# Kernel tuning notes

Hardware: AMD Instinct MI355X
Metric: run time of the kernel (lower is better)

Reference implementation:

```python
import jax, jax.numpy as jnp
import numpy as np

KERNEL = 5
PADDING = 2

def setup_inputs() -> dict:
    key = jax.random.key(0)
    k1, k2 = jax.random.split(key)
    x = jax.random.normal(k1, (16, 16, 512, 512), dtype=jnp.float32)
    filter_w = jax.random.normal(k2, (16, 16, KERNEL), dtype=jnp.float32)
    return {"x": x, "filter_w": filter_w}

def reference(x, filter_w):
    # torch.diag_embed: (C_out, C_in, k) -> (C_out, C_in, k, k) with values on the diagonal
    k = filter_w.shape[-1]
    kernel = filter_w[..., :, None] * jnp.eye(k, dtype=filter_w.dtype)  # OIHW
    out = jax.lax.conv_general_dilated(
        x, kernel,
        window_strides=(1, 1),
        padding=((PADDING, PADDING), (PADDING, PADDING)),
        dimension_numbers=("NCHW", "OIHW", "NCHW"),
    )
    return out
```

## Files before the change

### kernel.cpp

```cpp
#include <hip/hip_runtime.h>


#define HH    512
#define WW    512
#define CH    16
#define KK    5
#define IMG   (HH * WW)
#define CHIMG (CH * IMG)

#define HT 16
#define WT 64
#define RI 20
#define WI 68
#define NCHUNK (RI * 2)

typedef __attribute__((ext_vector_type(8))) short bf16x8;
typedef __attribute__((ext_vector_type(4))) float f32x4;
typedef __attribute__((ext_vector_type(4))) int   i32x4;

union I4S8 { i32x4 i; bf16x8 s; };

__device__ __forceinline__ unsigned cvt_pk_bf16(float lo, float hi) {
    unsigned r;
    asm("v_cvt_pk_bf16_f32 %0, %1, %2" : "=v"(r) : "v"(lo), "v"(hi));
    return r;
}

__global__ __launch_bounds__(256)
void diag_conv_mfma(const float* __restrict__ x,
                    const float* __restrict__ fw,
                    float* __restrict__ out)
{
    __shared__ i32x4 xl[NCHUNK * WI];

    const int tid = threadIdx.x;

    const int bid = blockIdx.x;
    const int swz = ((bid & 7) << 9) | (bid >> 3);
    const int n  = swz >> 8;
    const int ht = (swz >> 3) & 31;
    const int wt = swz & 7;
    const int h0 = ht * HT;
    const int w0 = wt * WT;

    const int wv   = tid >> 6;
    const int lane = tid & 63;

    const float* __restrict__ xn = x + (size_t)n * CHIMG;

#pragma unroll
    for (int u = 0; u < 10; ++u) {
        const int unit = u * 4 + wv;
        const int ri = unit >> 1;
        const int ih = unit & 1;
        const int r  = h0 - 2 + ri;
        const int w  = w0 - 2 + lane;
        const bool ok = ((unsigned)r < (unsigned)HH) & ((unsigned)w < (unsigned)WW);
        const int rc = r < 0 ? 0 : (r > HH - 1 ? HH - 1 : r);
        const int wc = w < 0 ? 0 : (w > WW - 1 ? WW - 1 : w);
        const float* __restrict__ p8 = xn + (size_t)(ih * 8) * IMG + (size_t)rc * WW + wc;
        float v0 = p8[0 * (size_t)IMG], v1 = p8[1 * (size_t)IMG];
        float v2 = p8[2 * (size_t)IMG], v3 = p8[3 * (size_t)IMG];
        float v4 = p8[4 * (size_t)IMG], v5 = p8[5 * (size_t)IMG];
        float v6 = p8[6 * (size_t)IMG], v7 = p8[7 * (size_t)IMG];
        if (!ok) { v0=v1=v2=v3=v4=v5=v6=v7 = 0.f; }
        i32x4 pk;
        pk.x = (int)cvt_pk_bf16(v0, v1);
        pk.y = (int)cvt_pk_bf16(v2, v3);
        pk.z = (int)cvt_pk_bf16(v4, v5);
        pk.w = (int)cvt_pk_bf16(v6, v7);
        xl[unit * WI + lane] = pk;
    }
    if (tid < 160) {
        const int ri  = tid >> 3;
        const int rem = tid & 7;
        const int wi  = 64 + (rem & 3);
        const int ih  = rem >> 2;
        const int r   = h0 - 2 + ri;
        const int w   = w0 - 2 + wi;
        const bool ok = ((unsigned)r < (unsigned)HH) & ((unsigned)w < (unsigned)WW);
        const int rc = r < 0 ? 0 : (r > HH - 1 ? HH - 1 : r);
        const int wc = w < 0 ? 0 : (w > WW - 1 ? WW - 1 : w);
        const float* __restrict__ p8 = xn + (size_t)(ih * 8) * IMG + (size_t)rc * WW + wc;
        float v0 = p8[0 * (size_t)IMG], v1 = p8[1 * (size_t)IMG];
        float v2 = p8[2 * (size_t)IMG], v3 = p8[3 * (size_t)IMG];
        float v4 = p8[4 * (size_t)IMG], v5 = p8[5 * (size_t)IMG];
        float v6 = p8[6 * (size_t)IMG], v7 = p8[7 * (size_t)IMG];
        if (!ok) { v0=v1=v2=v3=v4=v5=v6=v7 = 0.f; }
        i32x4 pk;
        pk.x = (int)cvt_pk_bf16(v0, v1);
        pk.y = (int)cvt_pk_bf16(v2, v3);
        pk.z = (int)cvt_pk_bf16(v4, v5);
        pk.w = (int)cvt_pk_bf16(v6, v7);
        xl[(ri * 2 + ih) * WI + wi] = pk;
    }

    const int p   = lane & 15;
    const int ihl = (lane >> 4) & 1;
    const int tb  = lane >> 5;

    bf16x8 afrag[3];
#pragma unroll
    for (int s = 0; s < 3; ++s) {
        const int tap = 2 * s + tb;
        I4S8 a;
        a.i = (i32x4){0, 0, 0, 0};
        if (tap < KK) {
            const float* __restrict__ wp = fw + ((size_t)p * CH + ihl * 8) * KK + tap;
            float q0 = wp[0 * KK], q1 = wp[1 * KK], q2 = wp[2 * KK], q3 = wp[3 * KK];
            float q4 = wp[4 * KK], q5 = wp[5 * KK], q6 = wp[6 * KK], q7 = wp[7 * KK];
            a.i.x = (int)cvt_pk_bf16(q0, q1);
            a.i.y = (int)cvt_pk_bf16(q2, q3);
            a.i.z = (int)cvt_pk_bf16(q4, q5);
            a.i.w = (int)cvt_pk_bf16(q6, q7);
        }
        afrag[s] = a.s;
    }

    __syncthreads();

    f32x4 acc[4][4];
#pragma unroll
    for (int yy = 0; yy < 4; ++yy)
#pragma unroll
        for (int g = 0; g < 4; ++g) acc[yy][g] = (f32x4){0.f, 0.f, 0.f, 0.f};

    const int ybase = wv * 4;
#pragma unroll
    for (int yy = 0; yy < 4; ++yy) {
#pragma unroll
        for (int s = 0; s < 3; ++s) {
            const int tap = 2 * s + tb;
            int ri = ybase + yy + tap;
            ri = ri > RI - 1 ? RI - 1 : ri;
            const int c = ri * 2 + ihl;
#pragma unroll
            for (int g = 0; g < 4; ++g) {
                int wi = g * 16 + p + tap;
                wi = wi > WI - 1 ? WI - 1 : wi;
                I4S8 b;
                b.i = xl[c * WI + wi];
                acc[yy][g] = __builtin_amdgcn_mfma_f32_16x16x32_bf16(
                    afrag[s], b.s, acc[yy][g], 0, 0, 0);
            }
        }
    }

    float* __restrict__ on = out + (size_t)n * CHIMG;
    const int og = (lane >> 4) << 2;
#pragma unroll
    for (int yy = 0; yy < 4; ++yy) {
        const int h = h0 + ybase + yy;
#pragma unroll
        for (int g = 0; g < 4; ++g) {
            const int wbase = w0 + g * 16 + p;
#pragma unroll
            for (int reg = 0; reg < 4; ++reg) {
                const int o = og + reg;
                on[(size_t)o * IMG + (size_t)h * WW + wbase] = acc[yy][g][reg];
            }
        }
    }
}

extern "C" void kernel_launch(void* const* d_in, const int* in_sizes, int n_in,
                              void* d_out, int out_size, void* d_ws, size_t ws_size,
                              hipStream_t stream)
{
    const float* x  = (const float*)d_in[0];
    const float* fw = (const float*)d_in[1];
    float* out      = (float*)d_out;

    diag_conv_mfma<<<dim3(4096), dim3(256), 0, stream>>>(x, fw, out);
}
```

Measured before the change: 157.0 us.

## Halve tile height, swap MFMA operands for vector stores, pad LDS, batch loads

The output tile height drops from 16 to 8 rows, doubling the grid to 8192 blocks and cutting per-block LDS and register use. The MFMA operands are swapped so each lane holds four consecutive output pixels, which allows 16-byte vector stores in place of scalar strided stores. LDS rows are padded to 69 chunks to reduce bank conflicts, and all global loads are issued before conversion to expose memory-level parallelism. The trade-off is more halo rows re-read per output row, since the 4 halo rows are now amortised over 8 rows instead of 16.

```diff
diff --git a/kernel.cpp b/kernel.cpp
--- a/kernel.cpp
+++ b/kernel.cpp
@@ -8,10 +8,11 @@
 #define IMG   (HH * WW)
 #define CHIMG (CH * IMG)
 
-#define HT 16
-#define WT 64
-#define RI 20
-#define WI 68
+#define HT  8
+#define WT  64
+#define RI  12
+#define WI  68
+#define WIP 69
 #define NCHUNK (RI * 2)
 
 typedef __attribute__((ext_vector_type(8))) short bf16x8;
@@ -31,14 +32,14 @@
                     const float* __restrict__ fw,
                     float* __restrict__ out)
 {
-    __shared__ i32x4 xl[NCHUNK * WI];
+    __shared__ i32x4 xl[NCHUNK * WIP];
 
     const int tid = threadIdx.x;
 
     const int bid = blockIdx.x;
-    const int swz = ((bid & 7) << 9) | (bid >> 3);
-    const int n  = swz >> 8;
-    const int ht = (swz >> 3) & 31;
+    const int swz = ((bid & 7) << 10) | (bid >> 3);
+    const int n  = swz >> 9;
+    const int ht = (swz >> 3) & 63;
     const int wt = swz & 7;
     const int h0 = ht * HT;
     const int w0 = wt * WT;
@@ -48,86 +49,97 @@
 
     const float* __restrict__ xn = x + (size_t)n * CHIMG;
 
+    const float* pu[6];
+    bool oku[6];
 #pragma unroll
-    for (int u = 0; u < 10; ++u) {
+    for (int u = 0; u < 6; ++u) {
         const int unit = u * 4 + wv;
         const int ri = unit >> 1;
         const int ih = unit & 1;
         const int r  = h0 - 2 + ri;
         const int w  = w0 - 2 + lane;
+        oku[u] = ((unsigned)r < (unsigned)HH) & ((unsigned)w < (unsigned)WW);
+        const int rc = r < 0 ? 0 : (r > HH - 1 ? HH - 1 : r);
+        const int wc = w < 0 ? 0 : (w > WW - 1 ? WW - 1 : w);
+        pu[u] = xn + (size_t)(ih * 8) * IMG + (size_t)rc * WW + wc;
+    }
+    float rv[6][8];
+#pragma unroll
+    for (int u = 0; u < 6; ++u)
+#pragma unroll
+        for (int j = 0; j < 8; ++j)
+            rv[u][j] = pu[u][(size_t)j * IMG];
+#pragma unroll
+    for (int u = 0; u < 6; ++u) {
+        const int unit = u * 4 + wv;
+        i32x4 pk;
+        if (!oku[u]) {
+#pragma unroll
+            for (int j = 0; j < 8; ++j) rv[u][j] = 0.f;
+        }
+        pk.x = (int)cvt_pk_bf16(rv[u][0], rv[u][1]);
+        pk.y = (int)cvt_pk_bf16(rv[u][2], rv[u][3]);
+        pk.z = (int)cvt_pk_bf16(rv[u][4], rv[u][5]);
+        pk.w = (int)cvt_pk_bf16(rv[u][6], rv[u][7]);
+        xl[unit * WIP + lane] = pk;
+    }
+    if (tid < 96) {
+        const int unit = tid >> 2;
+        const int wi   = 64 + (tid & 3);
+        const int ri = unit >> 1;
+        const int ih = unit & 1;
+        const int r  = h0 - 2 + ri;
+        const int w  = w0 - 2 + wi;
         const bool ok = ((unsigned)r < (unsigned)HH) & ((unsigned)w < (unsigned)WW);
         const int rc = r < 0 ? 0 : (r > HH - 1 ? HH - 1 : r);
         const int wc = w < 0 ? 0 : (w > WW - 1 ? WW - 1 : w);
         const float* __restrict__ p8 = xn + (size_t)(ih * 8) * IMG + (size_t)rc * WW + wc;
-        float v0 = p8[0 * (size_t)IMG], v1 = p8[1 * (size_t)IMG];
-        float v2 = p8[2 * (size_t)IMG], v3 = p8[3 * (size_t)IMG];
-        float v4 = p8[4 * (size_t)IMG], v5 = p8[5 * (size_t)IMG];
-        float v6 = p8[6 * (size_t)IMG], v7 = p8[7 * (size_t)IMG];
-        if (!ok) { v0=v1=v2=v3=v4=v5=v6=v7 = 0.f; }
+        float v[8];
+#pragma unroll
+        for (int j = 0; j < 8; ++j) v[j] = p8[(size_t)j * IMG];
+        if (!ok) {
+#pragma unroll
+            for (int j = 0; j < 8; ++j) v[j] = 0.f;
+        }
         i32x4 pk;
-        pk.x = (int)cvt_pk_bf16(v0, v1);
-        pk.y = (int)cvt_pk_bf16(v2, v3);
-        pk.z = (int)cvt_pk_bf16(v4, v5);
-        pk.w = (int)cvt_pk_bf16(v6, v7);
-        xl[unit * WI + lane] = pk;
-    }
-    if (tid < 160) {
-        const int ri  = tid >> 3;
-        const int rem = tid & 7;
-        const int wi  = 64 + (rem & 3);
-        const int ih  = rem >> 2;
-        const int r   = h0 - 2 + ri;
-        const int w   = w0 - 2 + wi;
-        const bool ok = ((unsigned)r < (unsigned)HH) & ((unsigned)w < (unsigned)WW);
-        const int rc = r < 0 ? 0 : (r > HH - 1 ? HH - 1 : r);
-        const int wc = w < 0 ? 0 : (w > WW - 1 ? WW - 1 : w);
-        const float* __restrict__ p8 = xn + (size_t)(ih * 8) * IMG + (size_t)rc * WW + wc;
-        float v0 = p8[0 * (size_t)IMG], v1 = p8[1 * (size_t)IMG];
-        float v2 = p8[2 * (size_t)IMG], v3 = p8[3 * (size_t)IMG];
-        float v4 = p8[4 * (size_t)IMG], v5 = p8[5 * (size_t)IMG];
-        float v6 = p8[6 * (size_t)IMG], v7 = p8[7 * (size_t)IMG];
-        if (!ok) { v0=v1=v2=v3=v4=v5=v6=v7 = 0.f; }
-        i32x4 pk;
-        pk.x = (int)cvt_pk_bf16(v0, v1);
-        pk.y = (int)cvt_pk_bf16(v2, v3);
-        pk.z = (int)cvt_pk_bf16(v4, v5);
-        pk.w = (int)cvt_pk_bf16(v6, v7);
-        xl[(ri * 2 + ih) * WI + wi] = pk;
+        pk.x = (int)cvt_pk_bf16(v[0], v[1]);
+        pk.y = (int)cvt_pk_bf16(v[2], v[3]);
+        pk.z = (int)cvt_pk_bf16(v[4], v[5]);
+        pk.w = (int)cvt_pk_bf16(v[6], v[7]);
+        xl[unit * WIP + wi] = pk;
     }
 
-    const int p   = lane & 15;
+    const int px  = lane & 15;
     const int ihl = (lane >> 4) & 1;
     const int tb  = lane >> 5;
 
-    bf16x8 afrag[3];
+    bf16x8 wfrag[3];
 #pragma unroll
     for (int s = 0; s < 3; ++s) {
         const int tap = 2 * s + tb;
         I4S8 a;
         a.i = (i32x4){0, 0, 0, 0};
         if (tap < KK) {
-            const float* __restrict__ wp = fw + ((size_t)p * CH + ihl * 8) * KK + tap;
-            float q0 = wp[0 * KK], q1 = wp[1 * KK], q2 = wp[2 * KK], q3 = wp[3 * KK];
-            float q4 = wp[4 * KK], q5 = wp[5 * KK], q6 = wp[6 * KK], q7 = wp[7 * KK];
-            a.i.x = (int)cvt_pk_bf16(q0, q1);
-            a.i.y = (int)cvt_pk_bf16(q2, q3);
-            a.i.z = (int)cvt_pk_bf16(q4, q5);
-            a.i.w = (int)cvt_pk_bf16(q6, q7);
+            const float* __restrict__ wp = fw + ((size_t)px * CH + ihl * 8) * KK + tap;
+            a.i.x = (int)cvt_pk_bf16(wp[0 * KK], wp[1 * KK]);
+            a.i.y = (int)cvt_pk_bf16(wp[2 * KK], wp[3 * KK]);
+            a.i.z = (int)cvt_pk_bf16(wp[4 * KK], wp[5 * KK]);
+            a.i.w = (int)cvt_pk_bf16(wp[6 * KK], wp[7 * KK]);
         }
-        afrag[s] = a.s;
+        wfrag[s] = a.s;
     }
 
     __syncthreads();
 
-    f32x4 acc[4][4];
+    f32x4 acc[2][4];
 #pragma unroll
-    for (int yy = 0; yy < 4; ++yy)
+    for (int yy = 0; yy < 2; ++yy)
 #pragma unroll
         for (int g = 0; g < 4; ++g) acc[yy][g] = (f32x4){0.f, 0.f, 0.f, 0.f};
 
-    const int ybase = wv * 4;
+    const int ybase = wv * 2;
 #pragma unroll
-    for (int yy = 0; yy < 4; ++yy) {
+    for (int yy = 0; yy < 2; ++yy) {
 #pragma unroll
         for (int s = 0; s < 3; ++s) {
             const int tap = 2 * s + tb;
@@ -136,29 +148,27 @@
             const int c = ri * 2 + ihl;
 #pragma unroll
             for (int g = 0; g < 4; ++g) {
-                int wi = g * 16 + p + tap;
+                int wi = g * 16 + px + tap;
                 wi = wi > WI - 1 ? WI - 1 : wi;
                 I4S8 b;
-                b.i = xl[c * WI + wi];
+                b.i = xl[c * WIP + wi];
                 acc[yy][g] = __builtin_amdgcn_mfma_f32_16x16x32_bf16(
-                    afrag[s], b.s, acc[yy][g], 0, 0, 0);
+                    b.s, wfrag[s], acc[yy][g], 0, 0, 0);
             }
         }
     }
 
     float* __restrict__ on = out + (size_t)n * CHIMG;
-    const int og = (lane >> 4) << 2;
+    const int o   = lane & 15;
+    const int pq  = (lane >> 4) << 2;
 #pragma unroll
-    for (int yy = 0; yy < 4; ++yy) {
+    for (int yy = 0; yy < 2; ++yy) {
         const int h = h0 + ybase + yy;
 #pragma unroll
         for (int g = 0; g < 4; ++g) {
-            const int wbase = w0 + g * 16 + p;
-#pragma unroll
-            for (int reg = 0; reg < 4; ++reg) {
-                const int o = og + reg;
-                on[(size_t)o * IMG + (size_t)h * WW + wbase] = acc[yy][g][reg];
-            }
+            float* __restrict__ dst =
+                on + (size_t)o * IMG + (size_t)h * WW + (w0 + g * 16 + pq);
+            *(f32x4*)dst = acc[yy][g];
         }
     }
 }
@@ -171,5 +181,5 @@
     const float* fw = (const float*)d_in[1];
     float* out      = (float*)d_out;
 
-    diag_conv_mfma<<<dim3(4096), dim3(256), 0, stream>>>(x, fw, out);
+    diag_conv_mfma<<<dim3(8192), dim3(256), 0, stream>>>(x, fw, out);
 }
```

Result: slower. 187.3 us (+19.3%).

## Repack input to padded NHWC bf16 workspace and convolve from global

Applied to the files above, without the earlier changes.

Adds a pre-pass that converts the NCHW fp32 input into a zero-padded NHWC bf16 buffer in the workspace. A second kernel then computes each output row with MFMAs, loading channel vectors directly from that buffer and skipping the shared-memory staging. The old kernel is kept as a fallback for when the workspace is too small. The fallback now swaps the MFMA operands so each lane stores four contiguous floats in one vector store. The repack costs an extra write and read of a large intermediate buffer in exchange for simpler, fully vectorized loads.

```diff
diff --git a/kernel.cpp b/kernel.cpp
--- a/kernel.cpp
+++ b/kernel.cpp
@@ -7,12 +7,9 @@
 #define KK    5
 #define IMG   (HH * WW)
 #define CHIMG (CH * IMG)
-
-#define HT 16
-#define WT 64
-#define RI 20
-#define WI 68
-#define NCHUNK (RI * 2)
+#define PH    517
+#define PIMG  (PH * PH)
+#define NEED_WS ((size_t)16 * PIMG * CH * 2)
 
 typedef __attribute__((ext_vector_type(8))) short bf16x8;
 typedef __attribute__((ext_vector_type(4))) float f32x4;
@@ -27,21 +24,121 @@
 }
 
 __global__ __launch_bounds__(256)
-void diag_conv_mfma(const float* __restrict__ x,
+void repack_nhwc_bf16(const float* __restrict__ x,
+                      unsigned short* __restrict__ ws)
+{
+    const int n  = blockIdx.y;
+    const int rp = blockIdx.x;
+    const int r  = rp - 2;
+    const bool rok = (unsigned)r < (unsigned)HH;
+
+    const float* __restrict__ xn = x + (size_t)n * CHIMG;
+    unsigned short* __restrict__ wrow =
+        ws + ((size_t)n * PIMG + (size_t)rp * PH) * CH;
+
+    for (int wp = threadIdx.x; wp < PH; wp += 256) {
+        const int w = wp - 2;
+        i32x4 lo = (i32x4){0, 0, 0, 0};
+        i32x4 hi = (i32x4){0, 0, 0, 0};
+        if (rok & ((unsigned)w < (unsigned)WW)) {
+            const float* __restrict__ p = xn + (size_t)r * WW + w;
+            float v[16];
+#pragma unroll
+            for (int c = 0; c < 16; ++c) v[c] = p[(size_t)c * IMG];
+            lo.x = (int)cvt_pk_bf16(v[0],  v[1]);
+            lo.y = (int)cvt_pk_bf16(v[2],  v[3]);
+            lo.z = (int)cvt_pk_bf16(v[4],  v[5]);
+            lo.w = (int)cvt_pk_bf16(v[6],  v[7]);
+            hi.x = (int)cvt_pk_bf16(v[8],  v[9]);
+            hi.y = (int)cvt_pk_bf16(v[10], v[11]);
+            hi.z = (int)cvt_pk_bf16(v[12], v[13]);
+            hi.w = (int)cvt_pk_bf16(v[14], v[15]);
+        }
+        *(i32x4*)(wrow + (size_t)wp * CH)     = lo;
+        *(i32x4*)(wrow + (size_t)wp * CH + 8) = hi;
+    }
+}
+
+__global__ __launch_bounds__(256)
+void conv_nhwc_mfma(const unsigned short* __restrict__ ws,
                     const float* __restrict__ fw,
                     float* __restrict__ out)
 {
-    __shared__ i32x4 xl[NCHUNK * WI];
+    const int bid = blockIdx.x;
+    const int swz = ((bid & 7) << 10) | (bid >> 3);
+    const int n = swz >> 9;
+    const int h = swz & 511;
+
+    const int tid  = threadIdx.x;
+    const int wv   = tid >> 6;
+    const int lane = tid & 63;
+    const int px   = lane & 15;
+    const int ihl  = (lane >> 4) & 1;
+    const int tb   = lane >> 5;
+
+    bf16x8 wfrag[3];
+#pragma unroll
+    for (int s = 0; s < 3; ++s) {
+        const int tap = 2 * s + tb;
+        I4S8 a;
+        a.i = (i32x4){0, 0, 0, 0};
+        if (tap < KK) {
+            const float* __restrict__ wp = fw + ((size_t)px * CH + ihl * 8) * KK + tap;
+            a.i.x = (int)cvt_pk_bf16(wp[0 * KK], wp[1 * KK]);
+            a.i.y = (int)cvt_pk_bf16(wp[2 * KK], wp[3 * KK]);
+            a.i.z = (int)cvt_pk_bf16(wp[4 * KK], wp[5 * KK]);
+            a.i.w = (int)cvt_pk_bf16(wp[6 * KK], wp[7 * KK]);
+        }
+        wfrag[s] = a.s;
+    }
+
+    const unsigned short* __restrict__ wsn = ws + (size_t)n * PIMG * CH;
+    int loff[3];
+#pragma unroll
+    for (int s = 0; s < 3; ++s) {
+        const int tap = 2 * s + tb;
+        loff[s] = ((h + tap) * PH + px + tap) * CH + ihl * 8;
+    }
+
+    float* __restrict__ outn = out + (size_t)n * CHIMG + (size_t)h * WW;
+    const int o  = lane & 15;
+    const int pq = (lane >> 4) << 2;
+
+#pragma unroll
+    for (int gi = 0; gi < 8; ++gi) {
+        const int g  = wv * 8 + gi;
+        const int cb = g * (16 * CH);
+        I4S8 a0, a1, a2;
+        a0.i = *(const i32x4*)(wsn + loff[0] + cb);
+        a1.i = *(const i32x4*)(wsn + loff[1] + cb);
+        a2.i = *(const i32x4*)(wsn + loff[2] + cb);
+        f32x4 acc = (f32x4){0.f, 0.f, 0.f, 0.f};
+        acc = __builtin_amdgcn_mfma_f32_16x16x32_bf16(a0.s, wfrag[0], acc, 0, 0, 0);
+        acc = __builtin_amdgcn_mfma_f32_16x16x32_bf16(a1.s, wfrag[1], acc, 0, 0, 0);
+        acc = __builtin_amdgcn_mfma_f32_16x16x32_bf16(a2.s, wfrag[2], acc, 0, 0, 0);
+        *(f32x4*)(outn + (size_t)o * IMG + g * 16 + pq) = acc;
+    }
+}
+
+#define F_RI 20
+#define F_WI 68
+#define F_NCHUNK 40
+
+__global__ __launch_bounds__(256)
+void fallback_r5(const float* __restrict__ x,
+                 const float* __restrict__ fw,
+                 float* __restrict__ out)
+{
+    __shared__ i32x4 xl[F_NCHUNK * F_WI];
 
     const int tid = threadIdx.x;
-
     const int bid = blockIdx.x;
     const int swz = ((bid & 7) << 9) | (bid >> 3);
     const int n  = swz >> 8;
     const int ht = (swz >> 3) & 31;
     const int wt = swz & 7;
-    const int h0 = ht * HT;
-    const int w0 = wt * WT;
+    const int h0 = ht * 16;
+    const int w0 = wt * 64;
 
     const int wv   = tid >> 6;
     const int lane = tid & 63;
@@ -69,7 +166,7 @@
         pk.y = (int)cvt_pk_bf16(v2, v3);
         pk.z = (int)cvt_pk_bf16(v4, v5);
         pk.w = (int)cvt_pk_bf16(v6, v7);
-        xl[unit * WI + lane] = pk;
+        xl[unit * F_WI + lane] = pk;
     }
     if (tid < 160) {
         const int ri  = tid >> 3;
@@ -92,10 +189,10 @@
         pk.y = (int)cvt_pk_bf16(v2, v3);
         pk.z = (int)cvt_pk_bf16(v4, v5);
         pk.w = (int)cvt_pk_bf16(v6, v7);
-        xl[(ri * 2 + ih) * WI + wi] = pk;
-    }
-
-    const int p   = lane & 15;
+        xl[(ri * 2 + ih) * F_WI + wi] = pk;
+    }
+
+    const int px  = lane & 15;
     const int ihl = (lane >> 4) & 1;
     const int tb  = lane >> 5;
 
@@ -106,13 +203,11 @@
         I4S8 a;
         a.i = (i32x4){0, 0, 0, 0};
         if (tap < KK) {
-            const float* __restrict__ wp = fw + ((size_t)p * CH + ihl * 8) * KK + tap;
-            float q0 = wp[0 * KK], q1 = wp[1 * KK], q2 = wp[2 * KK], q3 = wp[3 * KK];
-            float q4 = wp[4 * KK], q5 = wp[5 * KK], q6 = wp[6 * KK], q7 = wp[7 * KK];
-            a.i.x = (int)cvt_pk_bf16(q0, q1);
-            a.i.y = (int)cvt_pk_bf16(q2, q3);
-            a.i.z = (int)cvt_pk_bf16(q4, q5);
-            a.i.w = (int)cvt_pk_bf16(q6, q7);
+            const float* __restrict__ wp = fw + ((size_t)px * CH + ihl * 8) * KK + tap;
+            a.i.x = (int)cvt_pk_bf16(wp[0 * KK], wp[1 * KK]);
+            a.i.y = (int)cvt_pk_bf16(wp[2 * KK], wp[3 * KK]);
+            a.i.z = (int)cvt_pk_bf16(wp[4 * KK], wp[5 * KK]);
+            a.i.w = (int)cvt_pk_bf16(wp[6 * KK], wp[7 * KK]);
         }
         afrag[s] = a.s;
     }
@@ -132,33 +227,31 @@
         for (int s = 0; s < 3; ++s) {
             const int tap = 2 * s + tb;
             int ri = ybase + yy + tap;
-            ri = ri > RI - 1 ? RI - 1 : ri;
+            ri = ri > F_RI - 1 ? F_RI - 1 : ri;
             const int c = ri * 2 + ihl;
 #pragma unroll
             for (int g = 0; g < 4; ++g) {
-                int wi = g * 16 + p + tap;
-                wi = wi > WI - 1 ? WI - 1 : wi;
+                int wi = g * 16 + px + tap;
+                wi = wi > F_WI - 1 ? F_WI - 1 : wi;
                 I4S8 b;
-                b.i = xl[c * WI + wi];
+                b.i = xl[c * F_WI + wi];
                 acc[yy][g] = __builtin_amdgcn_mfma_f32_16x16x32_bf16(
-                    afrag[s], b.s, acc[yy][g], 0, 0, 0);
+                    b.s, afrag[s], acc[yy][g], 0, 0, 0);
             }
         }
     }
 
     float* __restrict__ on = out + (size_t)n * CHIMG;
-    const int og = (lane >> 4) << 2;
+    const int o  = lane & 15;
+    const int pq = (lane >> 4) << 2;
 #pragma unroll
     for (int yy = 0; yy < 4; ++yy) {
         const int h = h0 + ybase + yy;
 #pragma unroll
         for (int g = 0; g < 4; ++g) {
-            const int wbase = w0 + g * 16 + p;
-#pragma unroll
-            for (int reg = 0; reg < 4; ++reg) {
-                const int o = og + reg;
-                on[(size_t)o * IMG + (size_t)h * WW + wbase] = acc[yy][g][reg];
-            }
+            float* __restrict__ dst =
+                on + (size_t)o * IMG + (size_t)h * WW + (w0 + g * 16 + pq);
+            *(f32x4*)dst = acc[yy][g];
         }
     }
 }
@@ -171,5 +264,11 @@
     const float* fw = (const float*)d_in[1];
     float* out      = (float*)d_out;
 
-    diag_conv_mfma<<<dim3(4096), dim3(256), 0, stream>>>(x, fw, out);
-}
+    if (ws_size >= NEED_WS) {
+        unsigned short* ws = (unsigned short*)d_ws;
+        repack_nhwc_bf16<<<dim3(PH, 16), dim3(256), 0, stream>>>(x, ws);
+        conv_nhwc_mfma<<<dim3(8192), dim3(256), 0, stream>>>(ws, fw, out);
+    } else {
+        fallback_r5<<<dim3(4096), dim3(256), 0, stream>>>(x, fw, out);
+    }
+}
```

Result: slower. 286.9 us (+82.7%).

## Batch all global loads up front, swap MFMA operands for vectorized stores

Applied to the files above, without the earlier changes.

Issues every input and filter load before doing any conversion, using 32-bit offsets and a sched barrier, so the halo loads overlap instead of being serialized per unit. Swaps the MFMA A/B operands so each lane holds four consecutive output pixels of one channel, which lets the epilogue write one 16-byte vector store in place of four scalar strided stores. The trade-off is much higher register pressure from holding 80+ loaded floats live at once, which may reduce occupancy.

```diff
diff --git a/kernel.cpp b/kernel.cpp
--- a/kernel.cpp
+++ b/kernel.cpp
@@ -7,12 +7,8 @@
 #define KK    5
 #define IMG   (HH * WW)
 #define CHIMG (CH * IMG)
-
-#define HT 16
-#define WT 64
-#define RI 20
-#define WI 68
-#define NCHUNK (RI * 2)
+#define RI    20
+#define WI    68
 
 typedef __attribute__((ext_vector_type(8))) short bf16x8;
 typedef __attribute__((ext_vector_type(4))) float f32x4;
@@ -31,23 +27,40 @@
                     const float* __restrict__ fw,
                     float* __restrict__ out)
 {
-    __shared__ i32x4 xl[NCHUNK * WI];
+    __shared__ i32x4 xl[2 * RI * WI];
 
-    const int tid = threadIdx.x;
+    const int tid  = threadIdx.x;
+    const int wv   = tid >> 6;
+    const int lane = tid & 63;
 
     const int bid = blockIdx.x;
     const int swz = ((bid & 7) << 9) | (bid >> 3);
     const int n  = swz >> 8;
     const int ht = (swz >> 3) & 31;
     const int wt = swz & 7;
-    const int h0 = ht * HT;
-    const int w0 = wt * WT;
-
-    const int wv   = tid >> 6;
-    const int lane = tid & 63;
+    const int h0 = ht * 16;
+    const int w0 = wt * 64;
 
     const float* __restrict__ xn = x + (size_t)n * CHIMG;
 
+    const int px  = lane & 15;
+    const int ihl = (lane >> 4) & 1;
+    const int tb  = lane >> 5;
+
+    float wqv[3][8];
+    bool  wok[3];
+#pragma unroll
+    for (int s = 0; s < 3; ++s) {
+        const int tap = 2 * s + tb;
+        wok[s] = (tap < KK);
+        const float* __restrict__ wp =
+            fw + ((size_t)px * CH + ihl * 8) * KK + (wok[s] ? tap : 0);
+#pragma unroll
+        for (int q = 0; q < 8; ++q) wqv[s][q] = wp[q * KK];
+    }
+
+    unsigned off[10];
+    bool     oku[10];
 #pragma unroll
     for (int u = 0; u < 10; ++u) {
         const int unit = u * 4 + wv;
@@ -55,22 +68,21 @@
         const int ih = unit & 1;
         const int r  = h0 - 2 + ri;
         const int w  = w0 - 2 + lane;
-        const bool ok = ((unsigned)r < (unsigned)HH) & ((unsigned)w < (unsigned)WW);
+        oku[u] = ((unsigned)r < (unsigned)HH) & ((unsigned)w < (unsigned)WW);
         const int rc = r < 0 ? 0 : (r > HH - 1 ? HH - 1 : r);
         const int wc = w < 0 ? 0 : (w > WW - 1 ? WW - 1 : w);
-        const float* __restrict__ p8 = xn + (size_t)(ih * 8) * IMG + (size_t)rc * WW + wc;
-        float v0 = p8[0 * (size_t)IMG], v1 = p8[1 * (size_t)IMG];
-        float v2 = p8[2 * (size_t)IMG], v3 = p8[3 * (size_t)IMG];
-        float v4 = p8[4 * (size_t)IMG], v5 = p8[5 * (size_t)IMG];
-        float v6 = p8[6 * (size_t)IMG], v7 = p8[7 * (size_t)IMG];
-        if (!ok) { v0=v1=v2=v3=v4=v5=v6=v7 = 0.f; }
-        i32x4 pk;
-        pk.x = (int)cvt_pk_bf16(v0, v1);
-        pk.y = (int)cvt_pk_bf16(v2, v3);
-        pk.z = (int)cvt_pk_bf16(v4, v5);
-        pk.w = (int)cvt_pk_bf16(v6, v7);
-        xl[unit * WI + lane] = pk;
+        off[u] = (unsigned)(ih * 8 * IMG + rc * WW + wc);
     }
+    float rv[10][8];
+#pragma unroll
+    for (int u = 0; u < 10; ++u)
+#pragma unroll
+        for (int j = 0; j < 8; ++j)
+            rv[u][j] = xn[off[u] + (unsigned)(j * IMG)];
+
+    float tv[8];
+    bool  tok   = false;
+    int   tsite = 0;
     if (tid < 160) {
         const int ri  = tid >> 3;
         const int rem = tid & 7;
@@ -78,43 +90,51 @@
         const int ih  = rem >> 2;
         const int r   = h0 - 2 + ri;
         const int w   = w0 - 2 + wi;
-        const bool ok = ((unsigned)r < (unsigned)HH) & ((unsigned)w < (unsigned)WW);
+        tok = ((unsigned)r < (unsigned)HH) & ((unsigned)w < (unsigned)WW);
         const int rc = r < 0 ? 0 : (r > HH - 1 ? HH - 1 : r);
         const int wc = w < 0 ? 0 : (w > WW - 1 ? WW - 1 : w);
-        const float* __restrict__ p8 = xn + (size_t)(ih * 8) * IMG + (size_t)rc * WW + wc;
-        float v0 = p8[0 * (size_t)IMG], v1 = p8[1 * (size_t)IMG];
-        float v2 = p8[2 * (size_t)IMG], v3 = p8[3 * (size_t)IMG];
-        float v4 = p8[4 * (size_t)IMG], v5 = p8[5 * (size_t)IMG];
-        float v6 = p8[6 * (size_t)IMG], v7 = p8[7 * (size_t)IMG];
-        if (!ok) { v0=v1=v2=v3=v4=v5=v6=v7 = 0.f; }
-        i32x4 pk;
-        pk.x = (int)cvt_pk_bf16(v0, v1);
-        pk.y = (int)cvt_pk_bf16(v2, v3);
-        pk.z = (int)cvt_pk_bf16(v4, v5);
-        pk.w = (int)cvt_pk_bf16(v6, v7);
-        xl[(ri * 2 + ih) * WI + wi] = pk;
+        const unsigned toff = (unsigned)(ih * 8 * IMG + rc * WW + wc);
+        tsite = (ri * 2 + ih) * WI + wi;
+#pragma unroll
+        for (int j = 0; j < 8; ++j) tv[j] = xn[toff + (unsigned)(j * IMG)];
     }
 
-    const int p   = lane & 15;
-    const int ihl = (lane >> 4) & 1;
-    const int tb  = lane >> 5;
+    __builtin_amdgcn_sched_barrier(0);
 
     bf16x8 afrag[3];
 #pragma unroll
     for (int s = 0; s < 3; ++s) {
-        const int tap = 2 * s + tb;
         I4S8 a;
-        a.i = (i32x4){0, 0, 0, 0};
-        if (tap < KK) {
-            const float* __restrict__ wp = fw + ((size_t)p * CH + ihl * 8) * KK + tap;
-            float q0 = wp[0 * KK], q1 = wp[1 * KK], q2 = wp[2 * KK], q3 = wp[3 * KK];
-            float q4 = wp[4 * KK], q5 = wp[5 * KK], q6 = wp[6 * KK], q7 = wp[7 * KK];
-            a.i.x = (int)cvt_pk_bf16(q0, q1);
-            a.i.y = (int)cvt_pk_bf16(q2, q3);
-            a.i.z = (int)cvt_pk_bf16(q4, q5);
-            a.i.w = (int)cvt_pk_bf16(q6, q7);
-        }
+        a.i.x = (int)cvt_pk_bf16(wqv[s][0], wqv[s][1]);
+        a.i.y = (int)cvt_pk_bf16(wqv[s][2], wqv[s][3]);
+        a.i.z = (int)cvt_pk_bf16(wqv[s][4], wqv[s][5]);
+        a.i.w = (int)cvt_pk_bf16(wqv[s][6], wqv[s][7]);
+        if (!wok[s]) a.i = (i32x4){0, 0, 0, 0};
         afrag[s] = a.s;
+    }
+#pragma unroll
+    for (int u = 0; u < 10; ++u) {
+        const int unit = u * 4 + wv;
+        float v[8];
+#pragma unroll
+        for (int j = 0; j < 8; ++j) v[j] = oku[u] ? rv[u][j] : 0.f;
+        i32x4 pk;
+        pk.x = (int)cvt_pk_bf16(v[0], v[1]);
+        pk.y = (int)cvt_pk_bf16(v[2], v[3]);
+        pk.z = (int)cvt_pk_bf16(v[4], v[5]);
+        pk.w = (int)cvt_pk_bf16(v[6], v[7]);
+        xl[unit * WI + lane] = pk;
+    }
+    if (tid < 160) {
+        float v[8];
+#pragma unroll
+        for (int j = 0; j < 8; ++j) v[j] = tok ? tv[j] : 0.f;
+        i32x4 pk;
+        pk.x = (int)cvt_pk_bf16(v[0], v[1]);
+        pk.y = (int)cvt_pk_bf16(v[2], v[3]);
+        pk.z = (int)cvt_pk_bf16(v[4], v[5]);
+        pk.w = (int)cvt_pk_bf16(v[6], v[7]);
+        xl[tsite] = pk;
     }
 
     __syncthreads();
@@ -136,29 +156,27 @@
             const int c = ri * 2 + ihl;
 #pragma unroll
             for (int g = 0; g < 4; ++g) {
-                int wi = g * 16 + p + tap;
+                int wi = g * 16 + px + tap;
                 wi = wi > WI - 1 ? WI - 1 : wi;
                 I4S8 b;
                 b.i = xl[c * WI + wi];
                 acc[yy][g] = __builtin_amdgcn_mfma_f32_16x16x32_bf16(
-                    afrag[s], b.s, acc[yy][g], 0, 0, 0);
+                    b.s, afrag[s], acc[yy][g], 0, 0, 0);
             }
         }
     }
 
     float* __restrict__ on = out + (size_t)n * CHIMG;
-    const int og = (lane >> 4) << 2;
+    const int o  = lane & 15;
+    const int pq = (lane >> 4) << 2;
 #pragma unroll
     for (int yy = 0; yy < 4; ++yy) {
         const int h = h0 + ybase + yy;
 #pragma unroll
         for (int g = 0; g < 4; ++g) {
-            const int wbase = w0 + g * 16 + p;
-#pragma unroll
-            for (int reg = 0; reg < 4; ++reg) {
-                const int o = og + reg;
-                on[(size_t)o * IMG + (size_t)h * WW + wbase] = acc[yy][g][reg];
-            }
+            float* __restrict__ dst =
+                on + (size_t)o * IMG + (size_t)h * WW + (w0 + g * 16 + pq);
+            *(f32x4*)dst = acc[yy][g];
         }
     }
 }
```

After: 157.1 us. Within noise of the previous version (+0.0%).
